# Performance work log

Measured on AMD Instinct MI355X. Metric: run time of the kernel, lower is better.

The kernel has to match this reference:

```python
import jax, jax.numpy as jnp
import numpy as np

B, C, D, H, W = 2, 512, 32, 32, 32
L, CTX = 256, 768
NH, HD, G = 8, 64, 8
EPS = 1e-5


def group_norm(x, w, b):
    Bb, Cc, Dd, Hh, Ww = x.shape
    xg = x.reshape(Bb, G, Cc // G, Dd, Hh, Ww)
    mu = xg.mean(axis=(2, 3, 4, 5), keepdims=True)
    var = xg.var(axis=(2, 3, 4, 5), keepdims=True)
    xn = ((xg - mu) * jax.lax.rsqrt(var + EPS)).reshape(Bb, Cc, Dd, Hh, Ww)
    return xn * w[None, :, None, None, None] + b[None, :, None, None, None]


def layer_norm(x, w, b):
    mu = x.mean(axis=-1, keepdims=True)
    var = x.var(axis=-1, keepdims=True)
    return (x - mu) * jax.lax.rsqrt(var + EPS) * w + b


def setup_inputs() -> dict:
    key = jax.random.key(0)
    ks = jax.random.split(key, 8)
    s = 0.02  # weight init scale
    return {
        "x": jax.random.normal(ks[0], (B, C, D, H, W), jnp.float32),
        "context": jax.random.normal(ks[1], (B, L, CTX), jnp.float32),
        "gn_w": jnp.ones((C,), jnp.float32),
        "gn_b": jnp.zeros((C,), jnp.float32),
        "ln_w": jnp.ones((CTX,), jnp.float32),
        "ln_b": jnp.zeros((CTX,), jnp.float32),
        "q_w": jax.random.normal(ks[2], (C, C), jnp.float32) * s,
        "q_b": jnp.zeros((C,), jnp.float32),
        "k_w": jax.random.normal(ks[3], (C, CTX), jnp.float32) * s,
        "k_b": jnp.zeros((C,), jnp.float32),
        "v_w": jax.random.normal(ks[4], (C, CTX), jnp.float32) * s,
        "v_b": jnp.zeros((C,), jnp.float32),
        "proj_w": jax.random.normal(ks[5], (C, C), jnp.float32) * s,
        "proj_b": jnp.zeros((C,), jnp.float32),
    }


def reference(x, context, gn_w, gn_b, ln_w, ln_b, q_w, q_b, k_w, k_b, v_w, v_b, proj_w, proj_b):
    Bb, Cc, Dd, Hh, Ww = x.shape
    S = Dd * Hh * Ww
    h = group_norm(x, gn_w, gn_b)
    ctx = layer_norm(context, ln_w, ln_b)
    # 1x1 Conv3d == per-voxel linear over channels
    q = jnp.einsum('oc,bcdhw->bodhw', q_w, h) + q_b[None, :, None, None, None]
    q = q.reshape(Bb, NH, HD, S)                                        # (b,h,e,s)
    k = (ctx @ k_w.T + k_b).reshape(Bb, L, NH, HD).transpose(0, 2, 1, 3)  # (b,h,l,e)
    v = (ctx @ v_w.T + v_b).reshape(Bb, L, NH, HD).transpose(0, 2, 1, 3)  # (b,h,l,e)
    scale = HD ** -0.5
    attn = jnp.einsum('bhes,bhle->bhsl', q, k) * scale                  # (b,h,S,L)
    attn = jax.nn.softmax(attn, axis=-1)
    out = jnp.einsum('bhsl,bhle->bhes', attn, v).reshape(Bb, Cc, Dd, Hh, Ww)
    out = jnp.einsum('oc,bcdhw->bodhw', proj_w, out) + proj_b[None, :, None, None, None]
    return out + x
```

## Files before the change

kernel.cpp:

```cpp
#include <hip/hip_runtime.h>

typedef unsigned short u16;
typedef unsigned int u32;
typedef __attribute__((ext_vector_type(4))) float f32x4;
typedef __attribute__((ext_vector_type(8))) short bf16x8;
typedef __attribute__((ext_vector_type(8))) u16 u16x8;
typedef __attribute__((ext_vector_type(4))) u16 u16x4;
typedef __attribute__((ext_vector_type(4))) u32 u32x4;

#define DEVI __device__ __forceinline__

constexpr int C_ = 512, S_ = 32768, L_ = 256, CTX_ = 768;

DEVI u16 f2b(float f) {
    union { float f; unsigned u; } x; x.f = f;
    unsigned r = x.u + 0x7fffu + ((x.u >> 16) & 1u);
    return (u16)(r >> 16);
}

DEVI f32x4 mfma16(bf16x8 a, bf16x8 b, f32x4 c) {
    return __builtin_amdgcn_mfma_f32_16x16x32_bf16(a, b, c, 0, 0, 0);
}

DEVI void gload16(const void* g, void* l) {
    __builtin_amdgcn_global_load_lds(
        (const __attribute__((address_space(1))) void*)g,
        (__attribute__((address_space(3))) void*)l, 16, 0, 0);
}

DEVI u32 cvtpk(float lo, float hi) {
    u32 d;
    asm("v_cvt_pk_bf16_f32 %0, %1, %2" : "=v"(d) : "v"(lo), "v"(hi));
    return d;
}
DEVI void pl32(u32& a, u32& b) {
    asm volatile("v_permlane32_swap_b32 %0, %1" : "+v"(a), "+v"(b));
}
DEVI void pl16(u32& a, u32& b) {
    asm volatile("v_permlane16_swap_b32 %0, %1" : "+v"(a), "+v"(b));
}

__global__ __launch_bounds__(256) void cvt_w(
    const float* __restrict__ a0, const float* __restrict__ a1,
    const float* __restrict__ a2, const float* __restrict__ a3,
    u16* __restrict__ o0, u16* __restrict__ o1,
    u16* __restrict__ o2, u16* __restrict__ o3)
{
    int which = blockIdx.y;
    const float* src = which == 0 ? a0 : which == 1 ? a1 : which == 2 ? a2 : a3;
    u16* dst = which == 0 ? o0 : which == 1 ? o1 : which == 2 ? o2 : o3;
    int n4 = (which == 1 || which == 2) ? (512 * 768 / 4) : (512 * 512 / 4);
    int i = blockIdx.x * 256 + threadIdx.x;
    if (i < n4) {
        float4 v = ((const float4*)src)[i];
        u16x4 o; o[0] = f2b(v.x); o[1] = f2b(v.y); o[2] = f2b(v.z); o[3] = f2b(v.w);
        ((u16x4*)dst)[i] = o;
    }
}

__global__ __launch_bounds__(256) void gn_partial(const float* __restrict__ x,
                                                  float* __restrict__ part)
{
    const int bg = blockIdx.y, blk = blockIdx.x, tid = threadIdx.x;
    const float* base = x + (size_t)bg * 64 * S_ + (size_t)blk * 512;
    float s1 = 0.f, s2 = 0.f;
    for (int c = 0; c < 64; ++c) {
        const float* row = base + (size_t)c * S_;
        float v0 = row[tid], v1 = row[tid + 256];
        s1 += v0 + v1; s2 += v0 * v0 + v1 * v1;
    }
    for (int m = 1; m < 64; m <<= 1) { s1 += __shfl_xor(s1, m); s2 += __shfl_xor(s2, m); }
    __shared__ float a1[4], a2[4];
    int w = tid >> 6, lane = tid & 63;
    if (lane == 0) { a1[w] = s1; a2[w] = s2; }
    __syncthreads();
    if (tid == 0) {
        part[(bg * 64 + blk) * 2 + 0] = a1[0] + a1[1] + a1[2] + a1[3];
        part[(bg * 64 + blk) * 2 + 1] = a2[0] + a2[1] + a2[2] + a2[3];
    }
}

__global__ __launch_bounds__(64) void gn_final(const float* __restrict__ part,
                                               float* __restrict__ stats)
{
    int bg = blockIdx.x, tid = threadIdx.x;
    float s1 = part[(bg * 64 + tid) * 2], s2 = part[(bg * 64 + tid) * 2 + 1];
    for (int m = 1; m < 64; m <<= 1) { s1 += __shfl_xor(s1, m); s2 += __shfl_xor(s2, m); }
    if (tid == 0) {
        const float invN = 1.0f / (64.0f * (float)S_);
        float mu = s1 * invN, var = s2 * invN - mu * mu;
        stats[bg * 2] = mu;
        stats[bg * 2 + 1] = rsqrtf(var + 1e-5f);
    }
}

__global__ __launch_bounds__(256) void gn_apply(
    const float* __restrict__ x, const float* __restrict__ stats,
    const float* __restrict__ gw, const float* __restrict__ gb,
    u16* __restrict__ ht)
{
    __shared__ float tile[64][65];
    const int tid = threadIdx.x, sl = tid & 63, c4 = tid >> 6;
    const int s0 = blockIdx.x * 64, c0 = blockIdx.y * 64, b = blockIdx.z;
    const int bg = b * 8 + (c0 >> 6);
    const float mu = stats[bg * 2], rstd = stats[bg * 2 + 1];
#pragma unroll
    for (int i = 0; i < 16; ++i) {
        int cl = c4 * 16 + i;
        float wv = gw[c0 + cl], bv = gb[c0 + cl];
        float v = x[((size_t)(b * C_ + c0 + cl)) * S_ + s0 + sl];
        tile[sl][cl] = (v - mu) * rstd * wv + bv;
    }
    __syncthreads();
#pragma unroll
    for (int i = 0; i < 16; ++i) {
        int so = c4 * 16 + i;
        ht[((size_t)(b * S_ + s0 + so)) * C_ + c0 + sl] = f2b(tile[so][sl]);
    }
}

__global__ __launch_bounds__(256) void ln_ctx(
    const float* __restrict__ ctx, const float* __restrict__ lw,
    const float* __restrict__ lb, u16* __restrict__ cn)
{
    const int row = blockIdx.x, tid = threadIdx.x;
    const float* p = ctx + (size_t)row * CTX_;
    float v0 = p[tid], v1 = p[tid + 256], v2 = p[tid + 512];
    float s1 = v0 + v1 + v2, s2 = v0 * v0 + v1 * v1 + v2 * v2;
    for (int m = 1; m < 64; m <<= 1) { s1 += __shfl_xor(s1, m); s2 += __shfl_xor(s2, m); }
    __shared__ float a1[4], a2[4];
    int w = tid >> 6, lane = tid & 63;
    if (lane == 0) { a1[w] = s1; a2[w] = s2; }
    __syncthreads();
    s1 = a1[0] + a1[1] + a1[2] + a1[3];
    s2 = a2[0] + a2[1] + a2[2] + a2[3];
    const float invN = 1.0f / 768.0f;
    float mu = s1 * invN, rstd = rsqrtf(s2 * invN - mu * mu + 1e-5f);
    u16* o = cn + (size_t)row * CTX_;
    o[tid]       = f2b((v0 - mu) * rstd * lw[tid]       + lb[tid]);
    o[tid + 256] = f2b((v1 - mu) * rstd * lw[tid + 256] + lb[tid + 256]);
    o[tid + 512] = f2b((v2 - mu) * rstd * lw[tid + 512] + lb[tid + 512]);
}

template <int MODE>
__global__ __launch_bounds__(256, 2) void gemm_nt(
    const u16* __restrict__ A, const u16* __restrict__ Bp,
    const float* __restrict__ bias, void* __restrict__ outp,
    const float* __restrict__ resid, int K, int ldo,
    size_t aStride, size_t bStride, size_t oStride, float scale)
{
    __shared__ __align__(16) u16 lA[128 * 32];
    __shared__ __align__(16) u16 lB[128 * 32];
    const int tid = threadIdx.x;
    const int w = tid >> 6, lane = tid & 63;
    const int g = lane >> 4, r = lane & 15;
    const int m0 = blockIdx.x * 128, n0 = blockIdx.y * 128;
    const int z = blockIdx.z;
    A += (size_t)z * aStride;
    Bp += (size_t)z * bStride;

    const int srow = w * 32 + (lane >> 2);
    const int skc = (lane & 3) * 8;
    const int wr = w >> 1, wc = w & 1;

    f32x4 acc[4][4];
#pragma unroll
    for (int m = 0; m < 4; ++m)
#pragma unroll
        for (int n = 0; n < 4; ++n) acc[m][n] = f32x4{0.f, 0.f, 0.f, 0.f};

    for (int kt = 0; kt < K; kt += 32) {
        __syncthreads();
#pragma unroll
        for (int j = 0; j < 2; ++j) {
            int row = srow + j * 16;
            gload16(A + (size_t)(m0 + row) * K + kt + skc, &lA[(w * 32 + j * 16) * 32]);
            gload16(Bp + (size_t)(n0 + row) * K + kt + skc, &lB[(w * 32 + j * 16) * 32]);
        }
        __syncthreads();
        bf16x8 af[4], bf_[4];
#pragma unroll
        for (int m = 0; m < 4; ++m) af[m] = *(const bf16x8*)&lA[(wr * 64 + m * 16 + r) * 32 + g * 8];
#pragma unroll
        for (int n = 0; n < 4; ++n) bf_[n] = *(const bf16x8*)&lB[(wc * 64 + n * 16 + r) * 32 + g * 8];
#pragma unroll
        for (int m = 0; m < 4; ++m)
#pragma unroll
            for (int n = 0; n < 4; ++n)
                acc[m][n] = mfma16(af[m], bf_[n], acc[m][n]);
    }

    if constexpr (MODE == 0) {
        u16* ob = (u16*)outp + (size_t)z * oStride;
#pragma unroll
        for (int n = 0; n < 4; ++n) {
            int gn = n0 + wc * 64 + n * 16 + r;
            float bn = bias[gn] * scale;
#pragma unroll
            for (int m = 0; m < 4; ++m) {
                int gm = m0 + wr * 64 + m * 16 + g * 4;
#pragma unroll
                for (int i = 0; i < 4; ++i)
                    ob[(size_t)(gm + i) * ldo + gn] = f2b(acc[m][n][i] * scale + bn);
            }
        }
    } else if constexpr (MODE == 1) {
        u16* ob = (u16*)outp;
#pragma unroll
        for (int n = 0; n < 4; ++n) {
            int gn = n0 + wc * 64 + n * 16 + r;
            float bn = bias[gn];
#pragma unroll
            for (int m = 0; m < 4; ++m) {
                int gm = m0 + wr * 64 + m * 16 + g * 4;
                int bb = gm >> 8, l = gm & 255;
                u16x4 pk;
#pragma unroll
                for (int i = 0; i < 4; ++i) pk[i] = f2b(acc[m][n][i] + bn);
                *(u16x4*)&ob[((size_t)(bb * 512 + gn)) * 256 + l] = pk;
            }
        }
    } else {
        float* of = (float*)outp + (size_t)z * oStride;
        const float* rs = resid + (size_t)z * oStride;
#pragma unroll
        for (int m = 0; m < 4; ++m) {
            int gm = m0 + wr * 64 + m * 16 + g * 4;
#pragma unroll
            for (int i = 0; i < 4; ++i) {
                float bm = bias[gm + i];
#pragma unroll
                for (int n = 0; n < 4; ++n) {
                    int gn = n0 + wc * 64 + n * 16 + r;
                    size_t idx = (size_t)(gm + i) * ldo + gn;
                    of[idx] = acc[m][n][i] + bm + rs[idx];
                }
            }
        }
    }
}

__global__ __launch_bounds__(256, 2) void attn_kernel(
    const u16* __restrict__ q, const u16* __restrict__ kk,
    const u16* __restrict__ vv, u16* __restrict__ ao)
{
    __shared__ __align__(16) u16 sm[32768];
    const int tid = threadIdx.x;
    const int w = tid >> 6, lane = tid & 63;
    const int g = lane >> 4, r = lane & 15;
    const int bh = blockIdx.y, b = bh >> 3, h = bh & 7;
    const int s0 = blockIdx.x * 128;

    {
        const u16* kbase = kk + ((size_t)b * L_) * C_ + h * 64;
#pragma unroll
        for (int j = 0; j < 8; ++j) {
            int idx = j * 256 + tid;
            int l = idx >> 3, ch = idx & 7;
            u16x8 val = *(const u16x8*)(kbase + (size_t)l * C_ + ch * 8);
            *(u16x8*)&sm[l * 64 + ((ch ^ (l & 7)) << 3)] = val;
        }
        const u16* vbase = vv + ((size_t)bh * 64) * 256;
#pragma unroll
        for (int j = 0; j < 8; ++j) {
            int idx = j * 256 + tid;
            int e = idx >> 5, ch = idx & 31;
            u16x8 val = *(const u16x8*)(vbase + (size_t)e * 256 + ch * 8);
            *(u16x8*)&sm[16384 + e * 256 + ((ch ^ (e & 7)) << 3)] = val;
        }
    }

    const int sw = s0 + w * 32;
    bf16x8 qf[2][2];
#pragma unroll
    for (int m = 0; m < 2; ++m)
#pragma unroll
        for (int kt = 0; kt < 2; ++kt)
            qf[m][kt] = *(const bf16x8*)(q + ((size_t)(b * S_ + sw + m * 16 + r)) * C_
                                         + h * 64 + kt * 32 + g * 8);
    __syncthreads();

    f32x4 accs[2][16];
#pragma unroll
    for (int m = 0; m < 2; ++m)
#pragma unroll
        for (int n = 0; n < 16; ++n) accs[m][n] = f32x4{0.f, 0.f, 0.f, 0.f};
    __builtin_amdgcn_s_setprio(1);
#pragma unroll
    for (int n = 0; n < 16; ++n) {
#pragma unroll
        for (int kt = 0; kt < 2; ++kt) {
            int c = kt * 4 + g;
            bf16x8 kf = *(const bf16x8*)&sm[(n * 16 + r) * 64 + ((c ^ (r & 7)) << 3)];
#pragma unroll
            for (int m = 0; m < 2; ++m) accs[m][n] = mfma16(kf, qf[m][kt], accs[m][n]);
        }
    }
    __builtin_amdgcn_s_setprio(0);

    float inv[2];
#pragma unroll
    for (int m = 0; m < 2; ++m) {
        float mx = accs[m][0][0];
#pragma unroll
        for (int n = 0; n < 16; ++n)
#pragma unroll
            for (int i = 0; i < 4; ++i) mx = fmaxf(mx, accs[m][n][i]);
        mx = fmaxf(mx, __shfl_xor(mx, 16));
        mx = fmaxf(mx, __shfl_xor(mx, 32));
        float sum = 0.f;
#pragma unroll
        for (int n = 0; n < 16; ++n)
#pragma unroll
            for (int i = 0; i < 4; ++i) {
                float e = __expf(accs[m][n][i] - mx);
                accs[m][n][i] = e; sum += e;
            }
        sum += __shfl_xor(sum, 16);
        sum += __shfl_xor(sum, 32);
        inv[m] = 1.0f / sum;
    }

    f32x4 acco[2][4];
#pragma unroll
    for (int m = 0; m < 2; ++m)
#pragma unroll
        for (int n = 0; n < 4; ++n) acco[m][n] = f32x4{0.f, 0.f, 0.f, 0.f};

#pragma unroll
    for (int c = 0; c < 8; ++c) {
        bf16x8 pa[2];
#pragma unroll
        for (int m = 0; m < 2; ++m) {
            u32 x0 = cvtpk(accs[m][2 * c][0] * inv[m], accs[m][2 * c][1] * inv[m]);
            u32 x1 = cvtpk(accs[m][2 * c][2] * inv[m], accs[m][2 * c][3] * inv[m]);
            u32 y0 = cvtpk(accs[m][2 * c + 1][0] * inv[m], accs[m][2 * c + 1][1] * inv[m]);
            u32 y1 = cvtpk(accs[m][2 * c + 1][2] * inv[m], accs[m][2 * c + 1][3] * inv[m]);
            pl32(x0, y0);
            pl32(x1, y1);
            pl16(x0, y0);
            pl16(x1, y1);
            u32x4 pw; pw[0] = x0; pw[1] = x1; pw[2] = y0; pw[3] = y1;
            pa[m] = *(bf16x8*)&pw;
        }
        bf16x8 vf[4];
#pragma unroll
        for (int n = 0; n < 4; ++n) {
            int e = n * 16 + r;
            vf[n] = *(const bf16x8*)&sm[16384 + e * 256 + (((c * 4 + g) ^ (r & 7)) << 3)];
        }
        __builtin_amdgcn_s_setprio(1);
#pragma unroll
        for (int m = 0; m < 2; ++m)
#pragma unroll
            for (int n = 0; n < 4; ++n)
                acco[m][n] = mfma16(pa[m], vf[n], acco[m][n]);
        __builtin_amdgcn_s_setprio(0);
    }

#pragma unroll
    for (int m = 0; m < 2; ++m)
#pragma unroll
        for (int n = 0; n < 4; ++n)
#pragma unroll
            for (int i = 0; i < 4; ++i) {
                int s = sw + m * 16 + g * 4 + i;
                int e = n * 16 + r;
                ao[((size_t)(b * S_ + s)) * C_ + h * 64 + e] = f2b(acco[m][n][i]);
            }
}

extern "C" void kernel_launch(void* const* d_in, const int* in_sizes, int n_in,
                              void* d_out, int out_size, void* d_ws, size_t ws_size,
                              hipStream_t stream)
{
    (void)in_sizes; (void)n_in; (void)out_size; (void)ws_size;
    const float* x    = (const float*)d_in[0];
    const float* ctx  = (const float*)d_in[1];
    const float* gn_w = (const float*)d_in[2];
    const float* gn_b = (const float*)d_in[3];
    const float* ln_w = (const float*)d_in[4];
    const float* ln_b = (const float*)d_in[5];
    const float* q_w  = (const float*)d_in[6];
    const float* q_b  = (const float*)d_in[7];
    const float* k_w  = (const float*)d_in[8];
    const float* k_b  = (const float*)d_in[9];
    const float* v_w  = (const float*)d_in[10];
    const float* v_b  = (const float*)d_in[11];
    const float* p_w  = (const float*)d_in[12];
    const float* p_b  = (const float*)d_in[13];
    float* out = (float*)d_out;

    char* ws = (char*)d_ws;
    constexpr size_t WS_WQ   = 0;
    constexpr size_t WS_WK   = WS_WQ + (size_t)512 * 512 * 2;
    constexpr size_t WS_WV   = WS_WK + (size_t)512 * 768 * 2;
    constexpr size_t WS_WP   = WS_WV + (size_t)512 * 768 * 2;
    constexpr size_t WS_PART = WS_WP + (size_t)512 * 512 * 2;
    constexpr size_t WS_STAT = WS_PART + (size_t)16 * 64 * 2 * 4;
    constexpr size_t WS_CTXN = WS_STAT + 256;
    constexpr size_t WS_K    = WS_CTXN + (size_t)512 * 768 * 2;
    constexpr size_t WS_V    = WS_K + (size_t)2 * 8 * 256 * 64 * 2;
    constexpr size_t WS_Q    = WS_V + (size_t)2 * 8 * 256 * 64 * 2;
    constexpr size_t WS_H    = WS_Q + (size_t)2 * 32768 * 512 * 2;

    u16* wq = (u16*)(ws + WS_WQ);
    u16* wk = (u16*)(ws + WS_WK);
    u16* wv = (u16*)(ws + WS_WV);
    u16* wp = (u16*)(ws + WS_WP);
    float* part  = (float*)(ws + WS_PART);
    float* stats = (float*)(ws + WS_STAT);
    u16* ctxn = (u16*)(ws + WS_CTXN);
    u16* kt   = (u16*)(ws + WS_K);
    u16* vt   = (u16*)(ws + WS_V);
    u16* qt   = (u16*)(ws + WS_Q);
    u16* ht   = (u16*)(ws + WS_H);
    u16* ao   = ht;

    const size_t bsc = (size_t)S_ * C_;

    cvt_w<<<dim3(384, 4), 256, 0, stream>>>(q_w, k_w, v_w, p_w, wq, wk, wv, wp);
    gn_partial<<<dim3(64, 16), 256, 0, stream>>>(x, part);
    gn_final<<<16, 64, 0, stream>>>(part, stats);
    gn_apply<<<dim3(512, 8, 2), 256, 0, stream>>>(x, stats, gn_w, gn_b, ht);
    ln_ctx<<<512, 256, 0, stream>>>(ctx, ln_w, ln_b, ctxn);
    gemm_nt<0><<<dim3(256, 4, 2), 256, 0, stream>>>(ht, wq, q_b, qt, nullptr,
                                                    512, 512, bsc, 0, bsc, 0.125f);
    gemm_nt<0><<<dim3(4, 4, 1), 256, 0, stream>>>(ctxn, wk, k_b, kt, nullptr,
                                                  768, 512, 0, 0, 0, 1.0f);
    gemm_nt<1><<<dim3(4, 4, 1), 256, 0, stream>>>(ctxn, wv, v_b, vt, nullptr,
                                                  768, 0, 0, 0, 0, 1.0f);
    attn_kernel<<<dim3(256, 16), 256, 0, stream>>>(qt, kt, vt, ao);
    gemm_nt<2><<<dim3(4, 256, 2), 256, 0, stream>>>(wp, ao, p_b, out, x,
                                                    512, S_, 0, bsc, bsc, 1.0f);
}
```

Baseline: 307.8 us.

## Pipeline GEMM K-loop with 4-stage LDS ring, swizzle, and merge K/V launches

The GEMM main loop becomes a 4-buffer LDS ring with three tiles prefetched ahead. It uses explicit vmcnt waits and a single barrier per iteration instead of two syncthreads around each synchronous load. LDS rows are stored with an XOR swizzle to reduce bank conflicts on fragment reads. The K and V projection GEMMs are merged into one launch (MODE 3, z selects weight and output), saving a launch. LDS use grows to 64KB per block, which may limit occupancy to fewer than two blocks per CU.

Result: faster. 285.8 us (-7.2%).

```diff
diff --git a/kernel.cpp b/kernel.cpp
--- a/kernel.cpp
+++ b/kernel.cpp
@@ -147,21 +147,28 @@
     const u16* __restrict__ A, const u16* __restrict__ Bp,
     const float* __restrict__ bias, void* __restrict__ outp,
     const float* __restrict__ resid, int K, int ldo,
-    size_t aStride, size_t bStride, size_t oStride, float scale)
-{
-    __shared__ __align__(16) u16 lA[128 * 32];
-    __shared__ __align__(16) u16 lB[128 * 32];
+    size_t aStride, size_t bStride, size_t oStride, float scale,
+    const u16* __restrict__ Bp2, const float* __restrict__ bias2,
+    void* __restrict__ outp2)
+{
+    __shared__ __align__(16) u16 lA[4][4096];
+    __shared__ __align__(16) u16 lB[4][4096];
     const int tid = threadIdx.x;
     const int w = tid >> 6, lane = tid & 63;
     const int g = lane >> 4, r = lane & 15;
     const int m0 = blockIdx.x * 128, n0 = blockIdx.y * 128;
     const int z = blockIdx.z;
     A += (size_t)z * aStride;
-    Bp += (size_t)z * bStride;
-
-    const int srow = w * 32 + (lane >> 2);
-    const int skc = (lane & 3) * 8;
+    const u16* Bsel = Bp;
+    if constexpr (MODE == 3) { if (z) Bsel = Bp2; }
+    Bsel += (size_t)z * bStride;
+
+    const int l8 = lane & 7, lh = lane >> 3;
+    const int u_ = l8 ^ lh;
+    const int mro = (lh << 1) + (u_ >> 2);
+    const int kco = (u_ & 3) * 8;
     const int wr = w >> 1, wc = w & 1;
+    const int nt = K >> 5;
 
     f32x4 acc[4][4];
 #pragma unroll
@@ -169,26 +176,49 @@
 #pragma unroll
         for (int n = 0; n < 4; ++n) acc[m][n] = f32x4{0.f, 0.f, 0.f, 0.f};
 
-    for (int kt = 0; kt < K; kt += 32) {
-        __syncthreads();
-#pragma unroll
-        for (int j = 0; j < 2; ++j) {
-            int row = srow + j * 16;
-            gload16(A + (size_t)(m0 + row) * K + kt + skc, &lA[(w * 32 + j * 16) * 32]);
-            gload16(Bp + (size_t)(n0 + row) * K + kt + skc, &lB[(w * 32 + j * 16) * 32]);
-        }
-        __syncthreads();
+#define STAGE_T(t) {                                                           \
+    int bi_ = (t) & 3;                                                         \
+    size_t ko_ = (size_t)((t) * 32 + kco);                                     \
+    _Pragma("unroll")                                                          \
+    for (int j = 0; j < 2; ++j) {                                              \
+        int grow_ = w * 32 + j * 16 + mro;                                     \
+        gload16(A + (size_t)(m0 + grow_) * K + ko_,                            \
+                &lA[bi_][(w * 16 + j * 8) << 6]);                              \
+        gload16(Bsel + (size_t)(n0 + grow_) * K + ko_,                         \
+                &lB[bi_][(w * 16 + j * 8) << 6]);                              \
+    } }
+
+    STAGE_T(0); STAGE_T(1); STAGE_T(2);
+
+    for (int t = 0; t < nt; ++t) {
+        asm volatile("s_waitcnt lgkmcnt(0)" ::: "memory");
+        if (t < nt - 2)      asm volatile("s_waitcnt vmcnt(8)" ::: "memory");
+        else if (t == nt - 2) asm volatile("s_waitcnt vmcnt(4)" ::: "memory");
+        else                  asm volatile("s_waitcnt vmcnt(0)" ::: "memory");
+        __builtin_amdgcn_s_barrier();
+        asm volatile("" ::: "memory");
+        const int bi = t & 3;
         bf16x8 af[4], bf_[4];
 #pragma unroll
-        for (int m = 0; m < 4; ++m) af[m] = *(const bf16x8*)&lA[(wr * 64 + m * 16 + r) * 32 + g * 8];
-#pragma unroll
-        for (int n = 0; n < 4; ++n) bf_[n] = *(const bf16x8*)&lB[(wc * 64 + n * 16 + r) * 32 + g * 8];
+        for (int m = 0; m < 4; ++m) {
+            int row = wr * 32 + m * 8 + (r >> 1);
+            int slot = (((r & 1) << 2) + g) ^ ((r >> 1) & 7);
+            af[m] = *(const bf16x8*)&lA[bi][(row << 6) + (slot << 3)];
+        }
+#pragma unroll
+        for (int n = 0; n < 4; ++n) {
+            int row = wc * 32 + n * 8 + (r >> 1);
+            int slot = (((r & 1) << 2) + g) ^ ((r >> 1) & 7);
+            bf_[n] = *(const bf16x8*)&lB[bi][(row << 6) + (slot << 3)];
+        }
+        if (t + 3 < nt) STAGE_T(t + 3);
 #pragma unroll
         for (int m = 0; m < 4; ++m)
 #pragma unroll
             for (int n = 0; n < 4; ++n)
                 acc[m][n] = mfma16(af[m], bf_[n], acc[m][n]);
     }
+#undef STAGE_T
 
     if constexpr (MODE == 0) {
         u16* ob = (u16*)outp + (size_t)z * oStride;
@@ -204,23 +234,7 @@
                     ob[(size_t)(gm + i) * ldo + gn] = f2b(acc[m][n][i] * scale + bn);
             }
         }
-    } else if constexpr (MODE == 1) {
-        u16* ob = (u16*)outp;
-#pragma unroll
-        for (int n = 0; n < 4; ++n) {
-            int gn = n0 + wc * 64 + n * 16 + r;
-            float bn = bias[gn];
-#pragma unroll
-            for (int m = 0; m < 4; ++m) {
-                int gm = m0 + wr * 64 + m * 16 + g * 4;
-                int bb = gm >> 8, l = gm & 255;
-                u16x4 pk;
-#pragma unroll
-                for (int i = 0; i < 4; ++i) pk[i] = f2b(acc[m][n][i] + bn);
-                *(u16x4*)&ob[((size_t)(bb * 512 + gn)) * 256 + l] = pk;
-            }
-        }
-    } else {
+    } else if constexpr (MODE == 2) {
         float* of = (float*)outp + (size_t)z * oStride;
         const float* rs = resid + (size_t)z * oStride;
 #pragma unroll
@@ -234,6 +248,38 @@
                     int gn = n0 + wc * 64 + n * 16 + r;
                     size_t idx = (size_t)(gm + i) * ldo + gn;
                     of[idx] = acc[m][n][i] + bm + rs[idx];
+                }
+            }
+        }
+    } else if constexpr (MODE == 3) {
+        if (z == 0) {
+            u16* ob = (u16*)outp;
+#pragma unroll
+            for (int n = 0; n < 4; ++n) {
+                int gn = n0 + wc * 64 + n * 16 + r;
+                float bn = bias[gn];
+#pragma unroll
+                for (int m = 0; m < 4; ++m) {
+                    int gm = m0 + wr * 64 + m * 16 + g * 4;
+#pragma unroll
+                    for (int i = 0; i < 4; ++i)
+                        ob[(size_t)(gm + i) * ldo + gn] = f2b(acc[m][n][i] + bn);
+                }
+            }
+        } else {
+            u16* ob = (u16*)outp2;
+#pragma unroll
+            for (int n = 0; n < 4; ++n) {
+                int gn = n0 + wc * 64 + n * 16 + r;
+                float bn = bias2[gn];
+#pragma unroll
+                for (int m = 0; m < 4; ++m) {
+                    int gm = m0 + wr * 64 + m * 16 + g * 4;
+                    int bb = gm >> 8, l = gm & 255;
+                    u16x4 pk;
+#pragma unroll
+                    for (int i = 0; i < 4; ++i) pk[i] = f2b(acc[m][n][i] + bn);
+                    *(u16x4*)&ob[((size_t)(bb * 512 + gn)) * 256 + l] = pk;
                 }
             }
         }
@@ -425,12 +471,13 @@
     gn_apply<<<dim3(512, 8, 2), 256, 0, stream>>>(x, stats, gn_w, gn_b, ht);
     ln_ctx<<<512, 256, 0, stream>>>(ctx, ln_w, ln_b, ctxn);
     gemm_nt<0><<<dim3(256, 4, 2), 256, 0, stream>>>(ht, wq, q_b, qt, nullptr,
-                                                    512, 512, bsc, 0, bsc, 0.125f);
-    gemm_nt<0><<<dim3(4, 4, 1), 256, 0, stream>>>(ctxn, wk, k_b, kt, nullptr,
-                                                  768, 512, 0, 0, 0, 1.0f);
-    gemm_nt<1><<<dim3(4, 4, 1), 256, 0, stream>>>(ctxn, wv, v_b, vt, nullptr,
-                                                  768, 0, 0, 0, 0, 1.0f);
+                                                    512, 512, bsc, 0, bsc, 0.125f,
+                                                    nullptr, nullptr, nullptr);
+    gemm_nt<3><<<dim3(4, 4, 2), 256, 0, stream>>>(ctxn, wk, k_b, kt, nullptr,
+                                                  768, 512, 0, 0, 0, 1.0f,
+                                                  wv, v_b, vt);
     attn_kernel<<<dim3(256, 16), 256, 0, stream>>>(qt, kt, vt, ao);
     gemm_nt<2><<<dim3(4, 256, 2), 256, 0, stream>>>(wp, ao, p_b, out, x,
-                                                    512, S_, 0, bsc, bsc, 1.0f);
-}
+                                                    512, S_, 0, bsc, bsc, 1.0f,
+                                                    nullptr, nullptr, nullptr);
+}
```
